# Performance work log

Hardware: AMD Instinct MI355X
Metric: run time of the kernel (lower is better)

Reference implementation:

```python
import jax, jax.numpy as jnp
import numpy as np
from jax import lax

RATE = 2
KSIZE = 3
FUSE_K = 3
PAD = 1
SCALE = 10.0
ESCAPE_NAN = 1e-4
DN = ('NCHW', 'OIHW', 'NCHW')


def _patches(x, k, s, p):
    # x: [C,H,W] -> [L, C, k, k]  (matches torch pad + unfold(2).unfold(3) + permute)
    C = x.shape[0]
    pt = lax.conv_general_dilated_patches(
        x[None], (k, k), (s, s), [(p, p), (p, p)], dimension_numbers=DN)[0]
    oh, ow = pt.shape[1], pt.shape[2]
    # feature dim ordered (c, kh, kw)
    return pt.reshape(C, k, k, oh * ow).transpose(3, 0, 1, 2)


def setup_inputs() -> dict:
    key = jax.random.key(0)
    k1, k2 = jax.random.split(key)
    f = jax.random.normal(k1, (2, 128, 128, 128), dtype=jnp.float32)
    b = jax.random.normal(k2, (2, 128, 128, 128), dtype=jnp.float32)
    mask = jnp.zeros((1, 1, 128, 128), dtype=jnp.float32)
    return {"f": f, "b": b, "mask": mask}


def reference(f, b, mask):
    B, C, H, W = f.shape
    kernel = 2 * RATE  # 4
    # raw background patches (values for conv_transpose), per sample: [L, C, 4, 4]
    raw_w = jax.vmap(lambda bi: _patches(bi, kernel, RATE, PAD))(b)
    # nearest downsample by rate (torch nearest with scale 1/2 == strided slice)
    fd = f[:, :, ::RATE, ::RATE]
    bd = b[:, :, ::RATE, ::RATE]
    md = mask[:, :, ::RATE, ::RATE]
    fh, fw = fd.shape[2], fd.shape[3]
    bh, bw = bd.shape[2], bd.shape[3]
    L = bh * bw
    # matching (key) patches: [B, L, C, 3, 3]
    w = jax.vmap(lambda bi: _patches(bi, KSIZE, 1, PAD))(bd)
    # mask patches -> mm[l] = 1 where patch mean == 0 (valid background)
    m = _patches(md[0], KSIZE, 1, PAD)           # [L, 1, 3, 3]
    mm = (jnp.mean(m, axis=(1, 2, 3)) == 0.0).astype(f.dtype)[:, None, None]  # [L,1,1]

    fuse_w = jnp.eye(FUSE_K, dtype=f.dtype).reshape(1, 1, FUSE_K, FUSE_K)

    def fuse_conv(y):
        return lax.conv_general_dilated(y, fuse_w, (1, 1), [(1, 1), (1, 1)],
                                        dimension_numbers=DN)

    def one(xi, wi, rwi):
        # xi: [C,fh,fw], wi: [L,C,3,3], rwi: [L,C,4,4]
        norm = jnp.sqrt(jnp.sum(wi * wi, axis=(1, 2, 3), keepdims=True))
        wn = wi / jnp.maximum(norm, ESCAPE_NAN)
        # correlation scores (QK^T analogue): [1, L, fh, fw]
        yi = lax.conv_general_dilated(xi[None], wn, (1, 1), [(1, 1), (1, 1)],
                                      dimension_numbers=DN)
        # diagonal fuse convs, exactly mirroring the torch view/permute sequence
        yi = yi.reshape(1, 1, fh * fw, bh * bw)
        yi = fuse_conv(yi)
        yi = yi.reshape(fh, fw, bh, bw).transpose(1, 0, 3, 2).reshape(1, 1, fh * fw, bh * bw)
        yi = fuse_conv(yi)
        yi = yi.reshape(fw, fh, bw, bh).transpose(1, 0, 3, 2)  # [fh, fw, bh, bw]
        # faithful to the torch .view (plain contiguous reshape, no transpose)
        yi = yi.reshape(bh * bw, fh, fw)
        yi = yi * mm
        yi = jax.nn.softmax(yi * SCALE, axis=0) * mm
        # conv_transpose2d(yi, rwi, stride=rate, padding=1) / 4
        wt = jnp.flip(rwi, axis=(2, 3)).transpose(1, 0, 2, 3)  # [C, L, 4, 4]
        p = kernel - 1 - PAD  # 2
        out = lax.conv_general_dilated(yi[None], wt, (1, 1), [(p, p), (p, p)],
                                       lhs_dilation=(RATE, RATE),
                                       dimension_numbers=DN) / 4.0
        return out[0]  # [C, H, W]

    y = jax.vmap(one)(fd, w, raw_w)  # [B, C, H, W]
    return y
```

## Files before the change

kernel.cpp:

```cpp
#include <hip/hip_runtime.h>

#define CC 128
#define HH 128
#define WW 128
#define DH 64
#define DW 64
#define LTOT 4096
#define K0S 384
#define K2 2048
#define SCALE_F 10.0f
#define IMG ((size_t)CC * HH * WW)
#define PSTR 4104

typedef __attribute__((ext_vector_type(8))) short short8;
typedef __attribute__((ext_vector_type(4))) float f32x4;

struct Prep4 { const float* src[4]; unsigned short* dst[4]; float* ssq[4]; int lo[4]; };
struct PtrN2 { const float* ssq[2]; float* invn[2]; float* mmv[2]; };
struct PtrR2 { const float* src[2]; unsigned short* dst[2]; };

__device__ __forceinline__ unsigned short f2bf(float x) {
    union { float f; unsigned u; } v; v.f = x;
    unsigned r = v.u + 0x7fffu + ((v.u >> 16) & 1u);
    return (unsigned short)(r >> 16);
}
__device__ __forceinline__ float bf2f(unsigned short b) {
    union { unsigned u; float f; } v; v.u = ((unsigned)b) << 16;
    return v.f;
}

__device__ __forceinline__ f32x4 ld4u(const float* p) {
    f32x4 r; __builtin_memcpy(&r, p, 16); return r;
}

#define GLDS16(g, l) __builtin_amdgcn_global_load_lds( \
    (const __attribute__((address_space(1))) void*)(g), \
    (__attribute__((address_space(3))) void*)(l), 16, 0, 0)

__global__ __launch_bounds__(128) void split_ds_kernel(Prep4 P) {
    __shared__ float partial[2];
    int z = blockIdx.z;
    const float* __restrict__ src = P.src[z];
    unsigned short* __restrict__ dst = P.dst[z];
    int lo_in_seg1 = P.lo[z];
    int n = blockIdx.x;
    int c = threadIdx.x;
    int ny = n >> 6, nx = n & 63;
    float v = src[((size_t)c * HH + 2 * ny) * WW + 2 * nx];
    unsigned short hi = f2bf(v);
    unsigned short lo = f2bf(v - bf2f(hi));
    unsigned short* drow = dst + (size_t)n * K0S;
    drow[c]       = hi;
    drow[128 + c] = lo_in_seg1 ? lo : hi;
    drow[256 + c] = lo_in_seg1 ? hi : lo;

    float* ssq = P.ssq[z];
    if (ssq) {
        float s2 = v * v;
#pragma unroll
        for (int o = 32; o; o >>= 1) s2 += __shfl_xor(s2, o);
        if ((threadIdx.x & 63) == 0) partial[threadIdx.x >> 6] = s2;
        __syncthreads();
        if (threadIdx.x == 0) ssq[n] = partial[0] + partial[1];
    }
}

__global__ __launch_bounds__(256) void im2col_rawt_kernel(PtrR2 P) {
    int z = blockIdx.z;
    const float* __restrict__ src = P.src[z];
    unsigned short* __restrict__ dst = P.dst[z];
    int idx = blockIdx.x * 256 + threadIdx.x;
    int p = idx & (LTOT - 1);
    int m = idx >> 12;
    int px = p & 63, py = p >> 6;
    int ke = m & 3, kd = (m >> 2) & 3, c = m >> 4;
    int yy = 2 * py - 1 + kd, xx = 2 * px - 1 + ke;
    float v = 0.f;
    if (yy >= 0 && yy < HH && xx >= 0 && xx < WW)
        v = src[((size_t)c * HH + yy) * WW + xx];
    dst[idx] = f2bf(v);
}

__global__ void norm_mm_kernel(PtrN2 P, const float* __restrict__ mask) {
    int z = blockIdx.z;
    const float* __restrict__ ssq = P.ssq[z];
    float* __restrict__ inv_norm = P.invn[z];
    float* __restrict__ mmv = P.mmv[z];
    int p = blockIdx.x * blockDim.x + threadIdx.x;
    int px = p & 63, py = p >> 6;
    float s = 0.f, ms = 0.f;
    for (int di = -1; di <= 1; ++di)
        for (int dj = -1; dj <= 1; ++dj) {
            int y = py + di, x = px + dj;
            if (y >= 0 && y < DH && x >= 0 && x < DW) {
                s += ssq[y * 64 + x];
                ms += mask[(size_t)(2 * y) * WW + 2 * x];
            }
        }
    float n = sqrtf(s);
    if (n < 1e-4f) n = 1e-4f;
    inv_norm[p] = 1.f / n;
    mmv[p] = (ms == 0.f) ? 1.f : 0.f;
}

__global__ __launch_bounds__(256) void gemm_mfma(
    const unsigned short* __restrict__ Aop, const unsigned short* __restrict__ Bop,
    float* __restrict__ C, int M, int N, int K)
{
    __shared__ short As[128 * 64];
    __shared__ short Bs[128 * 64];
    int tid = threadIdx.x;
    int wave = tid >> 6, lane = tid & 63;
    int wm = (wave >> 1) * 64;
    int wn = (wave & 1) * 64;
    int bm = blockIdx.y * 128, bn = blockIdx.x * 128;

    int rowS = wave * 32;
    int lrow8 = lane >> 3;
    int gchunk = ((lane & 7) ^ lrow8) * 8;

    f32x4 acc[4][4] = {};

    int quad = lane >> 4;
    int r16 = lane & 15;
    int pc0 = ((quad)     ^ (r16 & 7)) * 8;
    int pc1 = ((4 + quad) ^ (r16 & 7)) * 8;

    const unsigned short* ap0 = Aop + (size_t)(bm + rowS +  0 + lrow8) * K + gchunk;
    const unsigned short* ap1 = Aop + (size_t)(bm + rowS +  8 + lrow8) * K + gchunk;
    const unsigned short* ap2 = Aop + (size_t)(bm + rowS + 16 + lrow8) * K + gchunk;
    const unsigned short* ap3 = Aop + (size_t)(bm + rowS + 24 + lrow8) * K + gchunk;
    const unsigned short* bp0 = Bop + (size_t)(bn + rowS +  0 + lrow8) * K + gchunk;
    const unsigned short* bp1 = Bop + (size_t)(bn + rowS +  8 + lrow8) * K + gchunk;
    const unsigned short* bp2 = Bop + (size_t)(bn + rowS + 16 + lrow8) * K + gchunk;
    const unsigned short* bp3 = Bop + (size_t)(bn + rowS + 24 + lrow8) * K + gchunk;
    short* lA = As + rowS * 64;
    short* lB = Bs + rowS * 64;

    for (int k0 = 0; k0 < K; k0 += 64) {
        GLDS16(ap0, lA);            GLDS16(ap1, lA + 8 * 64);
        GLDS16(ap2, lA + 16 * 64);  GLDS16(ap3, lA + 24 * 64);
        GLDS16(bp0, lB);            GLDS16(bp1, lB + 8 * 64);
        GLDS16(bp2, lB + 16 * 64);  GLDS16(bp3, lB + 24 * 64);
        ap0 += 64; ap1 += 64; ap2 += 64; ap3 += 64;
        bp0 += 64; bp1 += 64; bp2 += 64; bp3 += 64;
        __syncthreads();

        short8 a0[4], b0[4], a1[4], b1[4];
#pragma unroll
        for (int i = 0; i < 4; ++i) {
            a0[i] = *(const short8*)&As[(wm + i * 16 + r16) * 64 + pc0];
            b0[i] = *(const short8*)&Bs[(wn + i * 16 + r16) * 64 + pc0];
            a1[i] = *(const short8*)&As[(wm + i * 16 + r16) * 64 + pc1];
            b1[i] = *(const short8*)&Bs[(wn + i * 16 + r16) * 64 + pc1];
        }
#pragma unroll
        for (int i = 0; i < 4; ++i)
#pragma unroll
            for (int j = 0; j < 4; ++j) {
                acc[i][j] = __builtin_amdgcn_mfma_f32_16x16x32_bf16(a0[i], b0[j], acc[i][j], 0, 0, 0);
                acc[i][j] = __builtin_amdgcn_mfma_f32_16x16x32_bf16(a1[i], b1[j], acc[i][j], 0, 0, 0);
            }
        __syncthreads();
    }

    int col = lane & 15, rq = (lane >> 4) * 4;
#pragma unroll
    for (int i = 0; i < 4; ++i) {
#pragma unroll
        for (int r = 0; r < 4; ++r) {
            int m = bm + wm + i * 16 + rq + r;
#pragma unroll
            for (int j = 0; j < 4; ++j)
                C[(size_t)m * N + bn + wn + j * 16 + col] = acc[i][j][r];
        }
    }
}

__global__ __launch_bounds__(256) void stencil_norm_kernel(
    const float* __restrict__ C, const float* __restrict__ invn,
    float* __restrict__ Sg)
{
    int blk = blockIdx.x;
    int q = ((blk & 7) << 9) | (blk >> 3);
    int t = threadIdx.x;
    int qy = q >> 6, qx = q & 63;
    int chunk = t >> 2;
    int lanebase = (t & 3) << 4;
    int p0 = t << 4;

    f32x4 acc[4];
#pragma unroll
    for (int g = 0; g < 4; ++g) { acc[g][0] = acc[g][1] = acc[g][2] = acc[g][3] = 0.f; }

#pragma unroll
    for (int du = -1; du <= 1; ++du) {
        if (qy + du < 0 || qy + du > 63) continue;
        if (chunk + du < 0 || chunk + du > 63) continue;
#pragma unroll
        for (int dv = -1; dv <= 1; ++dv) {
            if (qx + dv < 0 || qx + dv > 63) continue;
            const float* rowp = C + (size_t)(q + 64 * du + dv) * LTOT + 64 * du + dv + p0;
#pragma unroll
            for (int g = 0; g < 4; ++g) {
                f32x4 lv = ld4u(rowp + 4 * g);
                if (dv == -1 && g == 0 && lanebase == 0)  lv[0] = 0.f;
                if (dv ==  1 && g == 3 && lanebase == 48) lv[3] = 0.f;
                acc[g] += lv;
            }
        }
    }
    float* orow = Sg + (size_t)q * PSTR;
#pragma unroll
    for (int g = 0; g < 4; ++g) {
        f32x4 iv = *(const f32x4*)(invn + p0 + 4 * g);
        *(f32x4*)(orow + p0 + 4 * g) = acc[g] * iv;
    }
    if (t == 0) { orow[-4] = orow[-3] = orow[-2] = orow[-1] = 0.f; }
    else if (t == 1) { orow[4096] = orow[4097] = orow[4098] = orow[4099] = 0.f; }
    if (q == 0) {
        float* gr = Sg - 4 - PSTR;
        for (int k = t; k < PSTR; k += 256) gr[k] = 0.f;
    }
    if (q == 4095) {
        float* gr = Sg - 4 + (size_t)4096 * PSTR;
        for (int k = t; k < PSTR; k += 256) gr[k] = 0.f;
    }
}

__global__ __launch_bounds__(256) void fused_conv_softmax_kernel(
    const float* __restrict__ Sg, const float* __restrict__ mmv,
    unsigned short* __restrict__ S16)
{
    __shared__ float redmax[4];
    __shared__ float redsum[4];
    int blk = blockIdx.x;
    int q = ((blk & 7) << 9) | (blk >> 3);
    int t = threadIdx.x;
    int lane = t & 63, wid = t >> 6;
    int chunk = t >> 2;
    int lanebase = (t & 3) << 4;
    int c0 = t << 4;

    int rbase = ((q & 63) << 6) | (q >> 6);

    f32x4 sacc[4];
#pragma unroll
    for (int g = 0; g < 4; ++g) { sacc[g][0] = sacc[g][1] = sacc[g][2] = sacc[g][3] = 0.f; }

#pragma unroll
    for (int j = 0; j < 3; ++j) {
        int r2 = rbase + (j - 1);
        if (r2 < 0 || r2 >= LTOT) continue;
        int rr = ((r2 & 63) << 6) | (r2 >> 6);
        int cj = chunk + (j - 1);
        int ccb;
        if (cj < 0)       ccb = 4031 + lanebase;
        else if (cj > 63) ccb = lanebase + 1;
        else              ccb = (cj << 6) + lanebase;
        const float* pr = Sg + (size_t)rr * PSTR + ccb;
#pragma unroll
        for (int g = 0; g < 4; ++g) {
            const float* pg = pr + 4 * g;
            f32x4 lm = ld4u(pg - (PSTR + 1));
            f32x4 l0 = ld4u(pg);
            f32x4 lp = ld4u(pg + (PSTR + 1));
            f32x4 tj = lm + l0 + lp;
            if (j == 0 && g == 0 && t == 0)   tj[0] = 0.f;
            if (j == 2 && g == 3 && t == 255) tj[3] = 0.f;
            sacc[g] += tj;
        }
    }

    float v[16];
#pragma unroll
    for (int g = 0; g < 4; ++g) {
        f32x4 m4 = *(const f32x4*)(mmv + c0 + 4 * g);
#pragma unroll
        for (int e = 0; e < 4; ++e)
            v[4 * g + e] = sacc[g][e] * m4[e] * SCALE_F;
    }
#pragma unroll
    for (int k = 0; k < 16; ++k) asm volatile("" : "+v"(v[k]));

    float mx = v[0];
#pragma unroll
    for (int i = 1; i < 16; ++i) mx = fmaxf(mx, v[i]);
#pragma unroll
    for (int o = 32; o; o >>= 1) mx = fmaxf(mx, __shfl_xor(mx, o));
    if (lane == 0) redmax[wid] = mx;
    __syncthreads();
    float gmx = fmaxf(fmaxf(redmax[0], redmax[1]), fmaxf(redmax[2], redmax[3]));

    float s = 0.f;
#pragma unroll
    for (int i = 0; i < 16; ++i) {
        v[i] = __expf(v[i] - gmx);
        s += v[i];
    }
#pragma unroll
    for (int o = 32; o; o >>= 1) s += __shfl_xor(s, o);
    if (lane == 0) redsum[wid] = s;
    __syncthreads();
    float inv = 1.f / (redsum[0] + redsum[1] + redsum[2] + redsum[3]);

    unsigned short* orow = S16 + (size_t)q * LTOT + c0;
    short8 h0, h1;
#pragma unroll
    for (int e = 0; e < 8; ++e) {
        h0[e] = (short)f2bf(v[e]     * inv * mmv[c0 + e]);
        h1[e] = (short)f2bf(v[8 + e] * inv * mmv[c0 + 8 + e]);
    }
    *(short8*)orow = h0;
    *(short8*)(orow + 8) = h1;
}

__global__ void output_kernel(const float* __restrict__ C2t, float* __restrict__ out) {
    int idx = blockIdx.x * blockDim.x + threadIdx.x;
    int x = idx & 127;
    int y = (idx >> 7) & 127;
    int c = idx >> 14;
    int oylo = max(0, (y - 1) >> 1), oyhi = min(63, (y + 1) >> 1);
    int oxlo = max(0, (x - 1) >> 1), oxhi = min(63, (x + 1) >> 1);
    float s = 0.f;
    for (int oy = oylo; oy <= oyhi; ++oy)
        for (int ox = oxlo; ox <= oxhi; ++ox) {
            int kd = y - 2 * oy + 1;
            int ke = x - 2 * ox + 1;
            s += C2t[(size_t)(c * 16 + kd * 4 + ke) * LTOT + oy * 64 + ox];
        }
    out[idx] = s * 0.25f;
}

extern "C" void kernel_launch(void* const* d_in, const int* in_sizes, int n_in,
                              void* d_out, int out_size, void* d_ws, size_t ws_size,
                              hipStream_t stream) {
    (void)in_sizes; (void)n_in; (void)out_size; (void)ws_size;
    const float* f    = (const float*)d_in[0];
    const float* b    = (const float*)d_in[1];
    const float* mask = (const float*)d_in[2];
    float* out = (float*)d_out;

    const size_t SZ_MAT  = (size_t)LTOT * LTOT * 4;
    const size_t SZ_SPAD = (size_t)PSTR * 4098 * 4;
    const size_t SZ_WR   = (size_t)K2 * LTOT * 2;
    const size_t SZ_SP   = (size_t)LTOT * K0S * 2;
    const size_t SZ_V    = (size_t)LTOT * 4;

    auto pad = [](size_t n) { return (n + 255) & ~(size_t)255; };
    char* p = (char*)d_ws;
    auto take = [&](size_t n) -> void* { void* r = (void*)p; p += pad(n); return r; };

    take(256);
    float* Buf1 = (float*)take(SZ_MAT);
    float* Spad = (float*)take(SZ_SPAD);
    unsigned short* W = (unsigned short*)take(SZ_WR);
    unsigned short* Bsp0 = (unsigned short*)take(SZ_SP);
    unsigned short* Fsp0 = (unsigned short*)take(SZ_SP);
    unsigned short* Bsp1 = (unsigned short*)take(SZ_SP);
    unsigned short* Fsp1 = (unsigned short*)take(SZ_SP);
    float* ssq0 = (float*)take(SZ_V);  float* ssq1 = (float*)take(SZ_V);
    float* invn0 = (float*)take(SZ_V); float* invn1 = (float*)take(SZ_V);
    float* mmv0 = (float*)take(SZ_V);  float* mmv1 = (float*)take(SZ_V);

    const float* f0 = f,  *b0 = b;
    const float* f1 = f + IMG, *b1 = b + IMG;

    float* Sg = Spad + PSTR + 4;
    unsigned short* S16 = (unsigned short*)Buf1;
    float* C2t = Spad;

    Prep4 P{{b0, f0, b1, f1}, {Bsp0, Fsp0, Bsp1, Fsp1},
            {ssq0, nullptr, ssq1, nullptr}, {1, 0, 1, 0}};
    split_ds_kernel<<<dim3(LTOT, 1, 4), 128, 0, stream>>>(P);
    PtrN2 nm{{ssq0, ssq1}, {invn0, invn1}, {mmv0, mmv1}};
    norm_mm_kernel<<<dim3(16, 1, 2), 256, 0, stream>>>(nm, mask);

    for (int bi = 0; bi < 2; ++bi) {
        const unsigned short* Fsp = bi ? Fsp1 : Fsp0;
        const unsigned short* Bsp = bi ? Bsp1 : Bsp0;
        const float* invn = bi ? invn1 : invn0;
        const float* mmv  = bi ? mmv1 : mmv0;

        PtrR2 rw{{bi ? b1 : b0, nullptr}, {W, nullptr}};
        im2col_rawt_kernel<<<dim3((size_t)K2 * LTOT / 256, 1, 1), 256, 0, stream>>>(rw);

        gemm_mfma<<<dim3(32, 32), 256, 0, stream>>>(Fsp, Bsp, Buf1, LTOT, LTOT, K0S);

        stencil_norm_kernel<<<LTOT, 256, 0, stream>>>(Buf1, invn, Sg);

        fused_conv_softmax_kernel<<<LTOT, 256, 0, stream>>>(Sg, mmv, S16);

        gemm_mfma<<<dim3(LTOT / 128, K2 / 128), 256, 0, stream>>>(W, S16, C2t, K2, LTOT, LTOT);

        output_kernel<<<CC * HH * WW / 256, 256, 0, stream>>>(C2t, out + (size_t)bi * IMG);
    }
}
```

Baseline: 547.3 us.

## Use triple-buffered 128x256 MFMA GEMM for the output contraction

Adds a new GEMM kernel for the second large matmul (K=4096). It uses 512 threads, 128x256 output tiles and a three-stage LDS ring filled by direct global-to-LDS loads, with explicit waitcnt and barrier control. Global loads are overlapped with the MFMA work, and s_setprio raises the priority of the compute phase. In exchange it uses much more LDS per block (about 144 KB) and runs fewer blocks, which could limit occupancy or load balance.

```diff
diff --git a/kernel.cpp b/kernel.cpp
--- a/kernel.cpp
+++ b/kernel.cpp
@@ -177,6 +177,93 @@
     }
 }
 
+__global__ __launch_bounds__(512, 2) void gemm_ring3(
+    const unsigned short* __restrict__ Aop, const unsigned short* __restrict__ Bop,
+    float* __restrict__ C, int N)
+{
+    constexpr int NT = 64;
+    constexpr int BUFS = (128 + 256) * 64;
+    __shared__ short lds[3 * BUFS];
+    const int K = NT * 64;
+    int tid = threadIdx.x;
+    int wave = tid >> 6, lane = tid & 63;
+    int wm = (wave >> 2) * 64;
+    int wn = (wave & 3) * 64;
+    int bm = blockIdx.y * 128, bn = blockIdx.x * 256;
+    int lrow8 = lane >> 3;
+    int gchunk = ((lane & 7) ^ lrow8) * 8;
+    int r16 = lane & 15, quad = lane >> 4;
+    int pc0 = ((quad)     ^ (r16 & 7)) * 8;
+    int pc1 = ((4 + quad) ^ (r16 & 7)) * 8;
+
+    const unsigned short* ap0 = Aop + (size_t)(bm + wave * 16 +  0 + lrow8) * K + gchunk;
+    const unsigned short* ap1 = Aop + (size_t)(bm + wave * 16 +  8 + lrow8) * K + gchunk;
+    const unsigned short* bp0 = Bop + (size_t)(bn + wave * 32 +  0 + lrow8) * K + gchunk;
+    const unsigned short* bp1 = Bop + (size_t)(bn + wave * 32 +  8 + lrow8) * K + gchunk;
+    const unsigned short* bp2 = Bop + (size_t)(bn + wave * 32 + 16 + lrow8) * K + gchunk;
+    const unsigned short* bp3 = Bop + (size_t)(bn + wave * 32 + 24 + lrow8) * K + gchunk;
+
+    f32x4 acc[4][4] = {};
+
+#define STAGE_T(s) do { \
+    short* la = lds + (s) * BUFS + (wave * 16) * 64; \
+    short* lb = lds + (s) * BUFS + 128 * 64 + (wave * 32) * 64; \
+    GLDS16(ap0, la); GLDS16(ap1, la + 8 * 64); \
+    GLDS16(bp0, lb); GLDS16(bp1, lb + 8 * 64); \
+    GLDS16(bp2, lb + 16 * 64); GLDS16(bp3, lb + 24 * 64); \
+    ap0 += 64; ap1 += 64; bp0 += 64; bp1 += 64; bp2 += 64; bp3 += 64; } while (0)
+
+    STAGE_T(0); STAGE_T(1); STAGE_T(2);
+    asm volatile("s_waitcnt vmcnt(12)" ::: "memory");
+    __builtin_amdgcn_s_barrier();
+    asm volatile("" ::: "memory");
+
+    int buf = 0;
+#pragma unroll 1
+    for (int T = 0; T < NT; ++T) {
+        const short* Ab = lds + buf * BUFS;
+        const short* Bb = Ab + 128 * 64;
+        short8 a0[4], a1[4], b0[4], b1[4];
+#pragma unroll
+        for (int i = 0; i < 4; ++i) {
+            a0[i] = *(const short8*)&Ab[(wm + i * 16 + r16) * 64 + pc0];
+            a1[i] = *(const short8*)&Ab[(wm + i * 16 + r16) * 64 + pc1];
+            b0[i] = *(const short8*)&Bb[(wn + i * 16 + r16) * 64 + pc0];
+            b1[i] = *(const short8*)&Bb[(wn + i * 16 + r16) * 64 + pc1];
+        }
+        asm volatile("s_waitcnt lgkmcnt(0)" ::: "memory");
+        __builtin_amdgcn_sched_barrier(0);
+        if (T + 2 < NT) { asm volatile("s_waitcnt vmcnt(6)" ::: "memory"); }
+        else            { asm volatile("s_waitcnt vmcnt(0)" ::: "memory"); }
+        __builtin_amdgcn_s_barrier();
+        asm volatile("" ::: "memory");
+        if (T + 3 < NT) STAGE_T(buf);
+        __builtin_amdgcn_s_setprio(1);
+#pragma unroll
+        for (int i = 0; i < 4; ++i)
+#pragma unroll
+            for (int j = 0; j < 4; ++j) {
+                acc[i][j] = __builtin_amdgcn_mfma_f32_16x16x32_bf16(a0[i], b0[j], acc[i][j], 0, 0, 0);
+                acc[i][j] = __builtin_amdgcn_mfma_f32_16x16x32_bf16(a1[i], b1[j], acc[i][j], 0, 0, 0);
+            }
+        __builtin_amdgcn_s_setprio(0);
+        buf = (buf == 2) ? 0 : buf + 1;
+    }
+#undef STAGE_T
+
+    int col = lane & 15, rq = (lane >> 4) * 4;
+#pragma unroll
+    for (int i = 0; i < 4; ++i) {
+#pragma unroll
+        for (int r = 0; r < 4; ++r) {
+            int m = bm + wm + i * 16 + rq + r;
+#pragma unroll
+            for (int j = 0; j < 4; ++j)
+                C[(size_t)m * N + bn + wn + j * 16 + col] = acc[i][j][r];
+        }
+    }
+}
+
 __global__ __launch_bounds__(256) void stencil_norm_kernel(
     const float* __restrict__ C, const float* __restrict__ invn,
     float* __restrict__ Sg)
@@ -391,7 +478,7 @@
 
         fused_conv_softmax_kernel<<<LTOT, 256, 0, stream>>>(Sg, mmv, S16);
 
-        gemm_mfma<<<dim3(LTOT / 128, K2 / 128), 256, 0, stream>>>(W, S16, C2t, K2, LTOT, LTOT);
+        gemm_ring3<<<dim3(LTOT / 256, K2 / 128), 512, 0, stream>>>(W, S16, C2t, LTOT);
 
         output_kernel<<<CC * HH * WW / 256, 256, 0, stream>>>(C2t, out + (size_t)bi * IMG);
     }
```

Result: faster. 518.0 us (-5.4%).
